# Kernel optimization log

Hardware: AMD Instinct MI355X
Metric: run time of the kernel (lower is better)

The kernel has to match this reference:

```python
import jax, jax.numpy as jnp
import numpy as np


def grid_sample_3d(vol, grid):
    """torch F.grid_sample 3D, mode='bilinear' (trilinear), align_corners=True.
    vol:  [B, C, Din, Hin, Win]
    grid: [B, Dout, Hout, Wout, 3] with xyz in [-1, 1] (x->W, y->H, z->D)
    returns [B, C, Dout, Hout, Wout]
    """
    B, C, Din, Hin, Win = vol.shape
    v = jnp.transpose(vol, (0, 2, 3, 4, 1))
    # align_corners=True: -1 -> 0, +1 -> size-1
    ix = (grid[..., 0] + 1.0) * 0.5 * (Win - 1)
    iy = (grid[..., 1] + 1.0) * 0.5 * (Hin - 1)
    iz = (grid[..., 2] + 1.0) * 0.5 * (Din - 1)
    x0 = jnp.floor(ix); y0 = jnp.floor(iy); z0 = jnp.floor(iz)
    wx = (ix - x0)[..., None]
    wy = (iy - y0)[..., None]
    wz = (iz - z0)[..., None]
    x0i = jnp.clip(x0.astype(jnp.int32), 0, Win - 1); x1i = jnp.clip(x0i + 1, 0, Win - 1)
    y0i = jnp.clip(y0.astype(jnp.int32), 0, Hin - 1); y1i = jnp.clip(y0i + 1, 0, Hin - 1)
    z0i = jnp.clip(z0.astype(jnp.int32), 0, Din - 1); z1i = jnp.clip(z0i + 1, 0, Din - 1)
    b = jnp.arange(B)[:, None, None, None]
    g = lambda z, y, x: v[b, z, y, x]  # [B, Dout, Hout, Wout, C]
    # interpolate along x, then y, then z
    c00 = g(z0i, y0i, x0i) * (1.0 - wx) + g(z0i, y0i, x1i) * wx
    c01 = g(z0i, y1i, x0i) * (1.0 - wx) + g(z0i, y1i, x1i) * wx
    c10 = g(z1i, y0i, x0i) * (1.0 - wx) + g(z1i, y0i, x1i) * wx
    c11 = g(z1i, y1i, x0i) * (1.0 - wx) + g(z1i, y1i, x1i) * wx
    c0 = c00 * (1.0 - wy) + c01 * wy
    c1 = c10 * (1.0 - wy) + c11 * wy
    out = c0 * (1.0 - wz) + c1 * wz  # [B, Dout, Hout, Wout, C]
    return jnp.transpose(out, (0, 4, 1, 2, 3))


def setup_inputs() -> dict:
    B, C, G, T = 2, 4, 128, 96
    key = jax.random.key(0)
    k1, k2, k3, k4 = jax.random.split(key, 4)
    grids = jax.random.uniform(k1, (B, G, G, G, 3), jnp.float32, minval=-1.0, maxval=1.0)
    deformation = jax.random.normal(k2, (B, 3, G, G, G), jnp.float32) * 0.1
    correction = jax.random.normal(k3, (B, C, G, G, G), jnp.float32) * 0.05
    template = jax.random.normal(k4, (B, C, T, T, T), jnp.float32)
    return {"grids": grids, "deformation": deformation, "correction": correction, "template": template}


def reference(grids, deformation, correction, template):
    # deformation: [B,3,W,H,D] -> [B,D,H,W,3]
    defp = jnp.transpose(deformation, (0, 4, 3, 2, 1))
    field = jnp.tanh(grids + defp)
    out = grid_sample_3d(template, field)           # [B,C,D,H,W]
    out = jnp.transpose(out, (0, 1, 4, 3, 2)) + correction  # [B,C,W,H,D]
    return (out, defp)
```

## Files before the change

### kernel.cpp

```cpp
#include <hip/hip_runtime.h>
#include <stdint.h>

#define G  128
#define TT 96
#define NB 2
#define NC 4
#define CS (TT * TT * TT)

typedef float f32x4 __attribute__((ext_vector_type(4)));
typedef float f32x2 __attribute__((ext_vector_type(2)));
typedef _Float16 f16x8 __attribute__((ext_vector_type(8)));
typedef _Float16 f16x8u __attribute__((ext_vector_type(8), aligned(8)));

__global__ __launch_bounds__(256) void tmpl_repack_f16(
        const float* __restrict__ tmpl, f16x8* __restrict__ out) {
    const int NP = NB * (CS / 2);
    int idx = blockIdx.x * 256 + threadIdx.x;
    if (idx >= NP) return;
    int b  = idx / (CS / 2);
    int s2 = idx - b * (CS / 2);
    const float* base = tmpl + (size_t)b * NC * CS + (size_t)s2 * 2;
    f16x8 o;
#pragma unroll
    for (int c = 0; c < NC; ++c) {
        f32x2 v = *(const f32x2*)(base + (size_t)c * CS);
        o[c]     = (_Float16)v.x;
        o[4 + c] = (_Float16)v.y;
    }
    out[idx] = o;
}

template <bool PACKED>
__global__ __launch_bounds__(256, 4) void fused_sample_kernel(
        const float* __restrict__ grids,
        const float* __restrict__ deform,
        const float* __restrict__ corr,
        const f16x8* __restrict__ tmpl_f16,
        const float* __restrict__ tmpl_raw,
        float* __restrict__ out2,
        float* __restrict__ defp) {
    __shared__ float lds[3][32][36];

    int blk = blockIdx.x;
    int wt = blk & 3;
    int dt = (blk >> 2) & 3;
    int h  = (blk >> 4) & 127;
    int b  = blk >> 11;
    int w0 = wt << 5, d0 = dt << 5;
    int tid = threadIdx.x;

    for (int idx = tid; idx < 768; idx += 256) {
        int c   = idx >> 8;
        int rem = idx & 255;
        int i   = rem >> 3;
        int j4  = (rem & 7) << 2;
        size_t off = ((((size_t)b * 3 + c) * G + (w0 + i)) * G + h) * G + (d0 + j4);
        f32x4 v = __builtin_nontemporal_load((const f32x4*)(deform + off));
        *(f32x4*)&lds[c][i][j4] = v;
    }
    __syncthreads();

    for (int idx = tid; idx < 768; idx += 256) {
        int j = idx / 24;
        int t = idx - j * 24;
        size_t off = (((((size_t)b * G + (d0 + j)) * G + h) * G + w0) * 3) + (size_t)t * 4;
        f32x4 gv = __builtin_nontemporal_load((const f32x4*)(grids + off));
        float dv[4];
#pragma unroll
        for (int k = 0; k < 4; ++k) {
            int e = t * 4 + k;
            int i = e / 3;
            int c = e - 3 * i;
            float d = lds[c][i][j];
            dv[k] = d;
            lds[c][i][j] = tanhf(gv[k] + d);
        }
        __builtin_nontemporal_store(*(f32x4*)dv, (f32x4*)(defp + off));
    }
    __syncthreads();

    const float SC = 0.5f * (TT - 1);
    const char* tb16 = (const char*)tmpl_f16 + (size_t)b * ((size_t)CS * 8);
    {
        int i  = tid >> 3;
        int j4 = (tid & 7) << 2;

        f32x4 fx = *(const f32x4*)&lds[0][i][j4];
        f32x4 fy = *(const f32x4*)&lds[1][i][j4];
        f32x4 fz = *(const f32x4*)&lds[2][i][j4];

        float wx[4], wy[4], wz[4];
        int base[4];
#pragma unroll
        for (int k = 0; k < 4; ++k) {
            float ix = (fx[k] + 1.0f) * SC;
            float iy = (fy[k] + 1.0f) * SC;
            float iz = (fz[k] + 1.0f) * SC;
            int x0 = min(max((int)floorf(ix), 0), TT - 2);
            int y0 = min(max((int)floorf(iy), 0), TT - 2);
            int z0 = min(max((int)floorf(iz), 0), TT - 2);
            wx[k] = ix - (float)x0;
            wy[k] = iy - (float)y0;
            wz[k] = iz - (float)z0;
            base[k] = (z0 * TT + y0) * TT + x0;
        }

        float r[4][4];
        if (PACKED) {
            f16x8 v00[4], v01[4], v10[4], v11[4];
#pragma unroll
            for (int k = 0; k < 4; ++k) {
                v00[k] = *(const f16x8u*)(tb16 + ((size_t)base[k]) * 8);
                v01[k] = *(const f16x8u*)(tb16 + ((size_t)(base[k] + TT)) * 8);
                v10[k] = *(const f16x8u*)(tb16 + ((size_t)(base[k] + TT * TT)) * 8);
                v11[k] = *(const f16x8u*)(tb16 + ((size_t)(base[k] + TT * TT + TT)) * 8);
            }
#pragma unroll
            for (int k = 0; k < 4; ++k) {
                float mx = 1.0f - wx[k], my = 1.0f - wy[k], mz = 1.0f - wz[k];
                float a00 = my * mz, a01 = wy[k] * mz;
                float a10 = my * wz[k], a11 = wy[k] * wz[k];
#pragma unroll
                for (int c = 0; c < NC; ++c) {
                    float t00 = (float)v00[k][c] * mx + (float)v00[k][4 + c] * wx[k];
                    float t01 = (float)v01[k][c] * mx + (float)v01[k][4 + c] * wx[k];
                    float t10 = (float)v10[k][c] * mx + (float)v10[k][4 + c] * wx[k];
                    float t11 = (float)v11[k][c] * mx + (float)v11[k][4 + c] * wx[k];
                    r[k][c] = t00 * a00 + t01 * a01 + t10 * a10 + t11 * a11;
                }
            }
        } else {
#pragma unroll
            for (int k = 0; k < 4; ++k) {
                float mx = 1.0f - wx[k], my = 1.0f - wy[k], mz = 1.0f - wz[k];
                float w000 = mx * my * mz, w001 = wx[k] * my * mz;
                float w010 = mx * wy[k] * mz, w011 = wx[k] * wy[k] * mz;
                float w100 = mx * my * wz[k], w101 = wx[k] * my * wz[k];
                float w110 = mx * wy[k] * wz[k], w111 = wx[k] * wy[k] * wz[k];
                size_t i000 = (size_t)base[k];
                size_t i001 = i000 + 1;
                size_t i010 = i000 + TT;
                size_t i011 = i010 + 1;
                size_t i100 = i000 + TT * TT;
                size_t i101 = i100 + 1;
                size_t i110 = i100 + TT;
                size_t i111 = i110 + 1;
#pragma unroll
                for (int c = 0; c < NC; ++c) {
                    const float* tb = tmpl_raw + ((size_t)b * NC + c) * CS;
                    r[k][c] = tb[i000]*w000 + tb[i001]*w001 + tb[i010]*w010 + tb[i011]*w011
                            + tb[i100]*w100 + tb[i101]*w101 + tb[i110]*w110 + tb[i111]*w111;
                }
            }
        }

        int w = w0 + i, d = d0 + j4;
        size_t obase = ((((size_t)b * NC) * (size_t)G + w) * G + h) * G + d;
        const size_t cstride = (size_t)G * G * G;
#pragma unroll
        for (int c = 0; c < NC; ++c) {
            f32x4 cv = __builtin_nontemporal_load((const f32x4*)(corr + obase + c * cstride));
            f32x4 ov;
            ov.x = r[0][c] + cv.x;
            ov.y = r[1][c] + cv.y;
            ov.z = r[2][c] + cv.z;
            ov.w = r[3][c] + cv.w;
            __builtin_nontemporal_store(ov, (f32x4*)(out2 + obase + c * cstride));
        }
    }
}

extern "C" void kernel_launch(void* const* d_in, const int* in_sizes, int n_in,
                              void* d_out, int out_size, void* d_ws, size_t ws_size,
                              hipStream_t stream) {
    const float* grids  = (const float*)d_in[0];
    const float* deform = (const float*)d_in[1];
    const float* corr   = (const float*)d_in[2];
    const float* tmpl   = (const float*)d_in[3];
    float* out2 = (float*)d_out;
    float* defp = out2 + (size_t)NB * NC * G * G * G;
    f16x8* tmpl_f16 = (f16x8*)d_ws;

    const size_t ws_needed = (size_t)NB * CS * 8;
    const bool packed = (ws_size >= ws_needed);

    if (packed) {
        int np = NB * (CS / 2);
        tmpl_repack_f16<<<(np + 255) / 256, 256, 0, stream>>>(tmpl, tmpl_f16);
    }

    int nblk = NB * G * 16;
    if (packed) {
        fused_sample_kernel<true><<<nblk, 256, 0, stream>>>(
            grids, deform, corr, tmpl_f16, tmpl, out2, defp);
    } else {
        fused_sample_kernel<false><<<nblk, 256, 0, stream>>>(
            grids, deform, corr, tmpl_f16, tmpl, out2, defp);
    }
}
```

Before: 333.3 us.

## Repack template into per-voxel 64-byte trilinear neighbor records

New measurement: 359.6 us. +7.9%, slower.

```diff
diff --git a/kernel.cpp b/kernel.cpp
--- a/kernel.cpp
+++ b/kernel.cpp
@@ -30,12 +30,46 @@
     out[idx] = o;
 }
 
-template <bool PACKED>
+__global__ __launch_bounds__(256) void tmpl_repack_rec64(
+        const float* __restrict__ tmpl, f16x8* __restrict__ out) {
+    const int NV = NB * CS;
+    int idx = blockIdx.x * 256 + threadIdx.x;
+    if (idx >= NV) return;
+    int b = idx / CS;
+    int s = idx - b * CS;
+    int x = s % TT;
+    int t = s / TT;
+    int y = t % TT;
+    int z = t / TT;
+    int x1 = min(x + 1, TT - 1);
+    int y1 = min(y + 1, TT - 1);
+    int z1 = min(z + 1, TT - 1);
+    const float* tb = tmpl + (size_t)b * NC * CS;
+    int zz[2] = {z, z1};
+    int yy[2] = {y, y1};
+    f16x8* dst = out + (size_t)idx * 4;
+#pragma unroll
+    for (int dz = 0; dz < 2; ++dz) {
+#pragma unroll
+        for (int dy = 0; dy < 2; ++dy) {
+            size_t p0 = ((size_t)zz[dz] * TT + yy[dy]) * TT;
+            f16x8 o;
+#pragma unroll
+            for (int c = 0; c < NC; ++c) {
+                o[c]     = (_Float16)tb[(size_t)c * CS + p0 + x];
+                o[4 + c] = (_Float16)tb[(size_t)c * CS + p0 + x1];
+            }
+            dst[dz * 2 + dy] = o;
+        }
+    }
+}
+
+template <int MODE>
 __global__ __launch_bounds__(256, 4) void fused_sample_kernel(
         const float* __restrict__ grids,
         const float* __restrict__ deform,
         const float* __restrict__ corr,
-        const f16x8* __restrict__ tmpl_f16,
+        const f16x8* __restrict__ tmpl_pk,
         const float* __restrict__ tmpl_raw,
         float* __restrict__ out2,
         float* __restrict__ defp) {
@@ -80,7 +114,6 @@
     __syncthreads();
 
     const float SC = 0.5f * (TT - 1);
-    const char* tb16 = (const char*)tmpl_f16 + (size_t)b * ((size_t)CS * 8);
     {
         int i  = tid >> 3;
         int j4 = (tid & 7) << 2;
@@ -106,14 +139,27 @@
         }
 
         float r[4][4];
-        if (PACKED) {
+        if (MODE >= 1) {
             f16x8 v00[4], v01[4], v10[4], v11[4];
-#pragma unroll
-            for (int k = 0; k < 4; ++k) {
-                v00[k] = *(const f16x8u*)(tb16 + ((size_t)base[k]) * 8);
-                v01[k] = *(const f16x8u*)(tb16 + ((size_t)(base[k] + TT)) * 8);
-                v10[k] = *(const f16x8u*)(tb16 + ((size_t)(base[k] + TT * TT)) * 8);
-                v11[k] = *(const f16x8u*)(tb16 + ((size_t)(base[k] + TT * TT + TT)) * 8);
+            if (MODE == 2) {
+                const char* tb64 = (const char*)tmpl_pk + (size_t)b * ((size_t)CS * 64);
+#pragma unroll
+                for (int k = 0; k < 4; ++k) {
+                    const f16x8* rec = (const f16x8*)(tb64 + (size_t)base[k] * 64);
+                    v00[k] = rec[0];
+                    v01[k] = rec[1];
+                    v10[k] = rec[2];
+                    v11[k] = rec[3];
+                }
+            } else {
+                const char* tb16 = (const char*)tmpl_pk + (size_t)b * ((size_t)CS * 8);
+#pragma unroll
+                for (int k = 0; k < 4; ++k) {
+                    v00[k] = *(const f16x8u*)(tb16 + ((size_t)base[k]) * 8);
+                    v01[k] = *(const f16x8u*)(tb16 + ((size_t)(base[k] + TT)) * 8);
+                    v10[k] = *(const f16x8u*)(tb16 + ((size_t)(base[k] + TT * TT)) * 8);
+                    v11[k] = *(const f16x8u*)(tb16 + ((size_t)(base[k] + TT * TT + TT)) * 8);
+                }
             }
 #pragma unroll
             for (int k = 0; k < 4; ++k) {
@@ -179,22 +225,25 @@
     const float* tmpl   = (const float*)d_in[3];
     float* out2 = (float*)d_out;
     float* defp = out2 + (size_t)NB * NC * G * G * G;
-    f16x8* tmpl_f16 = (f16x8*)d_ws;
-
-    const size_t ws_needed = (size_t)NB * CS * 8;
-    const bool packed = (ws_size >= ws_needed);
-
-    if (packed) {
+    f16x8* tmpl_pk = (f16x8*)d_ws;
+
+    const size_t ws2 = (size_t)NB * CS * 64;
+    const size_t ws1 = (size_t)NB * CS * 8;
+
+    int nblk = NB * G * 16;
+
+    if (ws_size >= ws2) {
+        int nv = NB * CS;
+        tmpl_repack_rec64<<<(nv + 255) / 256, 256, 0, stream>>>(tmpl, tmpl_pk);
+        fused_sample_kernel<2><<<nblk, 256, 0, stream>>>(
+            grids, deform, corr, tmpl_pk, tmpl, out2, defp);
+    } else if (ws_size >= ws1) {
         int np = NB * (CS / 2);
-        tmpl_repack_f16<<<(np + 255) / 256, 256, 0, stream>>>(tmpl, tmpl_f16);
-    }
-
-    int nblk = NB * G * 16;
-    if (packed) {
-        fused_sample_kernel<true><<<nblk, 256, 0, stream>>>(
-            grids, deform, corr, tmpl_f16, tmpl, out2, defp);
+        tmpl_repack_f16<<<(np + 255) / 256, 256, 0, stream>>>(tmpl, tmpl_pk);
+        fused_sample_kernel<1><<<nblk, 256, 0, stream>>>(
+            grids, deform, corr, tmpl_pk, tmpl, out2, defp);
     } else {
-        fused_sample_kernel<false><<<nblk, 256, 0, stream>>>(
-            grids, deform, corr, tmpl_f16, tmpl, out2, defp);
-    }
-}
+        fused_sample_kernel<0><<<nblk, 256, 0, stream>>>(
+            grids, deform, corr, tmpl_pk, tmpl, out2, defp);
+    }
+}
```
